# Kernel tuning notes

Hardware: AMD Instinct MI355X
Metric: run time of the kernel (lower is better)

## Reference

```python
import jax, jax.numpy as jnp
import numpy as np

N, E, G = 20000, 320000, 64
IN_DIM, HID, HEADS, NCLS = 512, 256, 2, 10
EPS = 1e-5
SLOPE = 0.2


def setup_inputs() -> dict:
    key = jax.random.key(0)
    ks = jax.random.split(key, 24)
    s = 0.02
    inp = {
        "feat": jax.random.normal(ks[0], (N, IN_DIM), jnp.float32),
        "src": jax.random.randint(ks[1], (E,), 0, N, jnp.int32),
        "dst": jax.random.randint(ks[2], (E,), 0, N, jnp.int32),
        "graph_ids": jnp.sort(jax.random.randint(ks[3], (N,), 0, G, jnp.int32)),
        # GATv2Conv params (fc_src, fc_dst, attn)
        "W_src": jax.random.normal(ks[4], (IN_DIM, HEADS * HID), jnp.float32) * s,
        "b_src": jnp.zeros((HEADS * HID,), jnp.float32),
        "W_dst": jax.random.normal(ks[5], (IN_DIM, HEADS * HID), jnp.float32) * s,
        "b_dst": jnp.zeros((HEADS * HID,), jnp.float32),
        "attn": jax.random.normal(ks[6], (HEADS, HID), jnp.float32) * s,
        # skip_lin: input_dim -> 2*hidden
        "W_skip": jax.random.normal(ks[7], (IN_DIM, 2 * HID), jnp.float32) * s,
        "b_skip": jnp.zeros((2 * HID,), jnp.float32),
        # bn1 affine
        "gamma": jnp.ones((2 * HID,), jnp.float32),
        "beta": jnp.zeros((2 * HID,), jnp.float32),
        # dim_reducer
        "W_red": jax.random.normal(ks[8], (2 * HID, HID), jnp.float32) * s,
        "b_red": jnp.zeros((HID,), jnp.float32),
        # attention-pool gate Linear(hidden, 1)
        "w_gate": jax.random.normal(ks[9], (HID, 1), jnp.float32) * s,
        "b_gate": jnp.zeros((1,), jnp.float32),
        # classifier MLP
        "W1": jax.random.normal(ks[10], (HID, HID // 2), jnp.float32) * s,
        "b1": jnp.zeros((HID // 2,), jnp.float32),
        "W2": jax.random.normal(ks[11], (HID // 2, NCLS), jnp.float32) * s,
        "b2": jnp.zeros((NCLS,), jnp.float32),
    }
    return inp


def _gatv2(feat, src, dst, W_src, b_src, W_dst, b_dst, attn):
    # feat_src/feat_dst: [N, H, D]
    fs = (feat @ W_src + b_src).reshape(N, HEADS, HID)
    fd = (feat @ W_dst + b_dst).reshape(N, HEADS, HID)
    fs_e = fs[src]                               # [E, H, D]
    m = jax.nn.leaky_relu(fs_e + fd[dst], SLOPE)  # [E, H, D]
    e = jnp.einsum("ehd,hd->eh", m, attn)         # [E, H]
    # edge softmax grouped by destination node
    e_max = jax.ops.segment_max(e, dst, num_segments=N)          # [N, H]
    e_exp = jnp.exp(e - e_max[dst])                               # [E, H]
    denom = jax.ops.segment_sum(e_exp, dst, num_segments=N)      # [N, H]
    alpha = e_exp / denom[dst]                                    # [E, H]
    out = jax.ops.segment_sum(alpha[:, :, None] * fs_e, dst, num_segments=N)
    return out  # [N, H, D]; zero rows for zero in-degree nodes


def reference(feat, src, dst, graph_ids, W_src, b_src, W_dst, b_dst, attn,
              W_skip, b_skip, gamma, beta, W_red, b_red, w_gate, b_gate,
              W1, b1, W2, b2):
    h1 = jax.nn.elu(_gatv2(feat, src, dst, W_src, b_src, W_dst, b_dst, attn))
    h1 = h1.reshape(N, HEADS * HID)
    h1 = h1 + (feat @ W_skip + b_skip)
    # BatchNorm1d (training-mode batch statistics, biased variance)
    mu = jnp.mean(h1, axis=0)
    var = jnp.mean((h1 - mu) ** 2, axis=0)
    h1 = (h1 - mu) * jax.lax.rsqrt(var + EPS) * gamma + beta
    hr = h1 @ W_red + b_red                      # [N, HID]
    # GlobalAttentionPooling: segment softmax of gate scores over each graph
    gate = hr @ w_gate + b_gate                  # [N, 1]
    g_max = jax.ops.segment_max(gate, graph_ids, num_segments=G)
    g_exp = jnp.exp(gate - g_max[graph_ids])
    g_den = jax.ops.segment_sum(g_exp, graph_ids, num_segments=G)
    a = g_exp / g_den[graph_ids]                 # [N, 1]
    h_g = jax.ops.segment_sum(a * hr, graph_ids, num_segments=G)  # [G, HID]
    # classifier (dropout = identity at inference)
    return jax.nn.relu(h_g @ W1 + b1) @ W2 + b2  # [G, NCLS]
```

## Files before the change

### kernel.cpp

```cpp
#include <hip/hip_runtime.h>
#include <math.h>

#define N_NODES 20000
#define N_EDGES 320000
#define N_GRAPH 64
#define IN_DIM  512
#define HID     256
#define F2      512
#define EPS_BN  1e-5f
#define SLOPE   0.2f
#define SCAN_BLOCKS 79
#define N_RT    157
#define RT_PAD  20096

#define SF_BLOCKS   5024
#define SW_BLOCKS   1024
#define INIT_BLOCKS 79
#define PREP_BLOCKS (SF_BLOCKS + SW_BLOCKS + INIT_BLOCKS)
#define TRIPLE_BLOCKS 1920
#define HIST_BLOCKS   1250

typedef unsigned short u16;
typedef __attribute__((ext_vector_type(8))) short bf16x8;
typedef __attribute__((ext_vector_type(4))) float floatx4;

__device__ __forceinline__ u16 bf_hi(float x) {
    unsigned int u = __float_as_uint(x);
    return (u16)((u + 0x7fffu + ((u >> 16) & 1u)) >> 16);
}
__device__ __forceinline__ float bf_val(u16 h) {
    return __uint_as_float((unsigned int)h << 16);
}
__device__ __forceinline__ void unpack2(unsigned int u, float& lo, float& hi) {
    lo = __uint_as_float(u << 16);
    hi = __uint_as_float(u & 0xffff0000u);
}
__device__ __forceinline__ float lr(float x) { return fmaxf(x, SLOPE * x); }

__global__ __launch_bounds__(256) void prep_kernel(
    const float* __restrict__ feat, u16* __restrict__ Fhi,
    const float* __restrict__ Ws, const float* __restrict__ Wd,
    const float* __restrict__ Wk, const float* __restrict__ Wr,
    u16* __restrict__ Whi, u16* __restrict__ Wlo,
    int* __restrict__ counts, int* __restrict__ cursor,
    float* __restrict__ stats, float* __restrict__ h_gnum,
    float* __restrict__ gden, float* __restrict__ gate) {
    __shared__ float t[32][33];
    int b = blockIdx.x;
    int tid = threadIdx.x;
    if (b < SF_BLOCKS) {
        int i = b * 256 + tid;
        size_t base = (size_t)i * 8;
        if (i >= N_NODES * IN_DIM / 8) {
            *(uint4*)(Fhi + base) = make_uint4(0, 0, 0, 0);
            return;
        }
        float4 x0 = *(const float4*)(feat + base);
        float4 x1 = *(const float4*)(feat + base + 4);
        float xs[8] = {x0.x, x0.y, x0.z, x0.w, x1.x, x1.y, x1.z, x1.w};
        union { u16 s[8]; uint4 v; } h;
#pragma unroll
        for (int j = 0; j < 8; j++) h.s[j] = bf_hi(xs[j]);
        *(uint4*)(Fhi + base) = h.v;
    } else if (b < SF_BLOCKS + SW_BLOCKS) {
        int bb = b - SF_BLOCKS;
        int kx = bb & 15, ny = (bb >> 4) & 15, w = bb >> 8;
        int ncols = (w == 3) ? 256 : 512;
        int n0 = ny * 32;
        if (n0 >= ncols) return;
        const float* W = (w == 0) ? Ws : ((w == 1) ? Wd : ((w == 2) ? Wk : Wr));
        size_t obase = (size_t)w * 512 * 512;
        int k0 = kx * 32;
        int tx = tid & 31, ty = tid >> 5;
#pragma unroll
        for (int i = 0; i < 4; i++)
            t[ty * 4 + i][tx] = W[(size_t)(k0 + ty * 4 + i) * ncols + n0 + tx];
        __syncthreads();
#pragma unroll
        for (int i = 0; i < 4; i++) {
            float x = t[tx][ty * 4 + i];
            u16 hh = bf_hi(x);
            size_t o = obase + (size_t)(n0 + ty * 4 + i) * 512 + k0 + tx;
            Whi[o] = hh;
            Wlo[o] = bf_hi(x - bf_val(hh));
        }
    } else {
        int i = (b - SF_BLOCKS - SW_BLOCKS) * 256 + tid;
        if (i < N_NODES) { counts[i] = 0; cursor[i] = 0; gate[i] = 0.f; }
        if (i < 1024) stats[i] = 0.f;
        if (i < N_GRAPH * HID) h_gnum[i] = 0.f;
        if (i < N_GRAPH) gden[i] = 0.f;
    }
}

__global__ __launch_bounds__(256) void gemm_mfma_triple(
    const u16* __restrict__ Fhi, const u16* __restrict__ Wthi,
    const float* __restrict__ b_src, const float* __restrict__ b_dst,
    const float* __restrict__ b_skip,
    u16* __restrict__ FS16, u16* __restrict__ FD16,
    u16* __restrict__ h1hi, u16* __restrict__ h1lo,
    const int* __restrict__ dst, int* __restrict__ counts) {
    __shared__ u16 As[2][128 * 72];
    int b = blockIdx.x;
    if (b >= TRIPLE_BLOCKS) {
        int e = (b - TRIPLE_BLOCKS) * 256 + threadIdx.x;
        if (e < N_EDGES) atomicAdd(&counts[dst[e]], 1);
        return;
    }
    int xcd = b & 7, slot = b >> 3;
    int rt = (slot / 12) * 8 + xcd;
    if (rt >= N_RT) return;
    int cw = slot % 12;
    int w_idx = cw >> 2;
    int col0 = (cw & 3) * 128;
    int row0 = rt * 128;
    int tid = threadIdx.x;
    int lane = tid & 63, wave = tid >> 6;
    int wm = (wave & 1) * 64, wn = (wave >> 1) * 64;
    int quad = lane >> 4, l16 = lane & 15;

    int sr = tid >> 1, sh = (tid & 1) * 32;
    const u16* gA = Fhi + (size_t)(row0 + sr) * 512 + sh;
    int sOff = sr * 72 + sh;

    const u16* Wb = Wthi + (size_t)w_idx * 512 * 512;
    const u16* bP[4];
#pragma unroll
    for (int nt = 0; nt < 4; nt++)
        bP[nt] = Wb + (size_t)(col0 + wn + nt * 16 + l16) * 512 + quad * 8;

    floatx4 acc[4][4];
#pragma unroll
    for (int i = 0; i < 4; i++)
#pragma unroll
        for (int j = 0; j < 4; j++) acc[i][j] = (floatx4){0.f, 0.f, 0.f, 0.f};

    union { uint4 u; bf16x8 v; } bcur[8], bnxt[8];
    {
        uint4 a0 = *(const uint4*)(gA + 0);
        uint4 a1 = *(const uint4*)(gA + 8);
        uint4 a2 = *(const uint4*)(gA + 16);
        uint4 a3 = *(const uint4*)(gA + 24);
#pragma unroll
        for (int nt = 0; nt < 4; nt++) {
            bcur[nt * 2 + 0].u = *(const uint4*)(bP[nt] + 0);
            bcur[nt * 2 + 1].u = *(const uint4*)(bP[nt] + 32);
        }
        *(uint4*)(&As[0][sOff + 0])  = a0;
        *(uint4*)(&As[0][sOff + 8])  = a1;
        *(uint4*)(&As[0][sOff + 16]) = a2;
        *(uint4*)(&As[0][sOff + 24]) = a3;
    }
    __syncthreads();

    for (int kk = 0; kk < 8; kk++) {
        uint4 na0, na1, na2, na3;
        bool more = kk < 7;
        if (more) {
            int k1 = (kk + 1) * 64;
            na0 = *(const uint4*)(gA + k1 + 0);
            na1 = *(const uint4*)(gA + k1 + 8);
            na2 = *(const uint4*)(gA + k1 + 16);
            na3 = *(const uint4*)(gA + k1 + 24);
#pragma unroll
            for (int nt = 0; nt < 4; nt++) {
                bnxt[nt * 2 + 0].u = *(const uint4*)(bP[nt] + k1 + 0);
                bnxt[nt * 2 + 1].u = *(const uint4*)(bP[nt] + k1 + 32);
            }
        }
        const u16* base = &As[kk & 1][0];
#pragma unroll
        for (int s = 0; s < 2; s++) {
#pragma unroll
            for (int mt = 0; mt < 4; mt++) {
                bf16x8 ah = *(const bf16x8*)&base[(wm + mt * 16 + l16) * 72 + s * 32 + quad * 8];
#pragma unroll
                for (int nt = 0; nt < 4; nt++)
                    acc[mt][nt] = __builtin_amdgcn_mfma_f32_16x16x32_bf16(
                        bcur[nt * 2 + s].v, ah, acc[mt][nt], 0, 0, 0);
            }
        }
        if (more) {
            u16* d = &As[(kk + 1) & 1][sOff];
            *(uint4*)(d + 0)  = na0;
            *(uint4*)(d + 8)  = na1;
            *(uint4*)(d + 16) = na2;
            *(uint4*)(d + 24) = na3;
            __syncthreads();
#pragma unroll
            for (int i = 0; i < 8; i++) bcur[i] = bnxt[i];
        }
    }

    const float* bias = (w_idx == 0) ? b_src : ((w_idx == 1) ? b_dst : b_skip);
    float4 b4[4];
#pragma unroll
    for (int wt = 0; wt < 4; wt++)
        b4[wt] = *(const float4*)(bias + col0 + wn + wt * 16 + quad * 4);
#pragma unroll
    for (int ft = 0; ft < 4; ft++) {
        int m = row0 + wm + ft * 16 + l16;
        if (m >= N_NODES) continue;
        size_t rb = (size_t)m * 512;
#pragma unroll
        for (int wt = 0; wt < 4; wt++) {
            int nb = col0 + wn + wt * 16 + quad * 4;
            float v0 = acc[ft][wt][0] + b4[wt].x;
            float v1 = acc[ft][wt][1] + b4[wt].y;
            float v2 = acc[ft][wt][2] + b4[wt].z;
            float v3 = acc[ft][wt][3] + b4[wt].w;
            u16 h0 = bf_hi(v0), h1_ = bf_hi(v1), h2 = bf_hi(v2), h3 = bf_hi(v3);
            uint2 wv;
            wv.x = (unsigned)h0 | ((unsigned)h1_ << 16);
            wv.y = (unsigned)h2 | ((unsigned)h3 << 16);
            if (w_idx == 0)      *(uint2*)(FS16 + rb + nb) = wv;
            else if (w_idx == 1) *(uint2*)(FD16 + rb + nb) = wv;
            else {
                *(uint2*)(h1hi + rb + nb) = wv;
                uint2 lv;
                lv.x = (unsigned)bf_hi(v0 - bf_val(h0)) | ((unsigned)bf_hi(v1 - bf_val(h1_)) << 16);
                lv.y = (unsigned)bf_hi(v2 - bf_val(h2)) | ((unsigned)bf_hi(v3 - bf_val(h3)) << 16);
                *(uint2*)(h1lo + rb + nb) = lv;
            }
        }
    }
}

__global__ __launch_bounds__(256) void scan_local_kernel(
    const int* __restrict__ counts, int* __restrict__ row_ptr, int* __restrict__ bsum) {
    __shared__ int buf[256];
    int b = blockIdx.x, tid = threadIdx.x;
    int i = b * 256 + tid;
    buf[tid] = (i < N_NODES) ? counts[i] : 0;
    __syncthreads();
    for (int off = 1; off < 256; off <<= 1) {
        int t = (tid >= off) ? buf[tid - off] : 0;
        __syncthreads();
        buf[tid] += t;
        __syncthreads();
    }
    if (i < N_NODES) row_ptr[i + 1] = buf[tid];
    if (tid == 255) bsum[b] = buf[255];
}

__global__ __launch_bounds__(256) void scan_fixup_kernel(
    const int* __restrict__ bsum, int* __restrict__ row_ptr) {
    __shared__ int red[256];
    int b = blockIdx.x, tid = threadIdx.x;
    red[tid] = (tid < b) ? bsum[tid] : 0;
    __syncthreads();
    for (int off = 128; off > 0; off >>= 1) {
        if (tid < off) red[tid] += red[tid + off];
        __syncthreads();
    }
    int offset = red[0];
    int i = b * 256 + tid;
    if (i < N_NODES) row_ptr[i + 1] += offset;
    if (b == 0 && tid == 0) row_ptr[0] = 0;
}

__global__ void scatter_kernel(const int* __restrict__ src, const int* __restrict__ dst,
                               const int* __restrict__ row_ptr,
                               int* __restrict__ cursor, int* __restrict__ csr_src) {
    int e = blockIdx.x * blockDim.x + threadIdx.x;
    if (e < N_EDGES) {
        int d = dst[e];
        int pos = atomicAdd(&cursor[d], 1);
        csr_src[row_ptr[d] + pos] = src[e];
    }
}

__global__ __launch_bounds__(256) void edge_fused_kernel(
    const u16* __restrict__ FS16, const u16* __restrict__ FD16,
    const float* __restrict__ attn, const int* __restrict__ csr_src,
    const int* __restrict__ row_ptr,
    u16* __restrict__ h1hi, u16* __restrict__ h1lo) {
    __shared__ float red[3 * 512];
    __shared__ float den[2];
    int n = blockIdx.x, tid = threadIdx.x;
    int lane = tid & 63, wave = tid >> 6;
    int beg = row_ptr[n], end = row_ptr[n + 1], deg = end - beg;
    if (tid < 2) den[tid] = 0.f;

    float fdv[8], aw[8];
    {
        uint4 q = *(const uint4*)(FD16 + (size_t)n * 512 + 8 * lane);
        unpack2(q.x, fdv[0], fdv[1]); unpack2(q.y, fdv[2], fdv[3]);
        unpack2(q.z, fdv[4], fdv[5]); unpack2(q.w, fdv[6], fdv[7]);
        float4 a0 = *(const float4*)(attn + 8 * lane);
        float4 a1 = *(const float4*)(attn + 8 * lane + 4);
        aw[0] = a0.x; aw[1] = a0.y; aw[2] = a0.z; aw[3] = a0.w;
        aw[4] = a1.x; aw[5] = a1.y; aw[6] = a1.z; aw[7] = a1.w;
    }
    __syncthreads();

    float acc[8] = {0.f, 0.f, 0.f, 0.f, 0.f, 0.f, 0.f, 0.f};
    float dp = 0.f;
    for (int j = wave; j < deg; j += 4) {
        int s = csr_src[beg + j];
        uint4 q = *(const uint4*)(FS16 + (size_t)s * 512 + 8 * lane);
        float f[8];
        unpack2(q.x, f[0], f[1]); unpack2(q.y, f[2], f[3]);
        unpack2(q.z, f[4], f[5]); unpack2(q.w, f[6], f[7]);
        float p = 0.f;
#pragma unroll
        for (int k = 0; k < 8; k++) p += lr(f[k] + fdv[k]) * aw[k];
#pragma unroll
        for (int off = 16; off > 0; off >>= 1) p += __shfl_xor(p, off, 64);
        float ex = expf(p);
#pragma unroll
        for (int k = 0; k < 8; k++) acc[k] += ex * f[k];
        if ((lane & 31) == 0) dp += ex;
    }
    if ((lane & 31) == 0) atomicAdd(&den[lane >> 5], dp);

    if (wave > 0) {
        float* r = &red[(wave - 1) * 512 + lane * 8];
        *(float4*)(r + 0) = *(float4*)&acc[0];
        *(float4*)(r + 4) = *(float4*)&acc[4];
    }
    __syncthreads();
    if (wave == 0) {
#pragma unroll
        for (int w = 0; w < 3; w++) {
            const float* r = &red[w * 512 + lane * 8];
#pragma unroll
            for (int k = 0; k < 8; k++) acc[k] += r[k];
        }
        float d = (lane < 32) ? den[0] : den[1];
        float inv = d > 0.f ? 1.f / d : 0.f;
        size_t base = (size_t)n * 512 + 8 * lane;
        union { u16 s[8]; uint4 v; } qh, ql;
        qh.v = *(const uint4*)(h1hi + base);
        ql.v = *(const uint4*)(h1lo + base);
#pragma unroll
        for (int k = 0; k < 8; k++) {
            float skip = bf_val(qh.s[k]) + bf_val(ql.s[k]);
            float x = acc[k] * inv;
            x = x > 0.f ? x : expm1f(x);
            float y = x + skip;
            u16 hh = bf_hi(y);
            qh.s[k] = hh;
            ql.s[k] = bf_hi(y - bf_val(hh));
        }
        *(uint4*)(h1hi + base) = qh.v;
        *(uint4*)(h1lo + base) = ql.v;
    }
}

__global__ __launch_bounds__(256) void bn_stats_kernel(const u16* __restrict__ h1hi,
                                                       float* __restrict__ stats,
                                                       int rows_per_block) {
    int tid = threadIdx.x;
    int r0 = blockIdx.x * rows_per_block;
    int r1 = min(r0 + rows_per_block, N_NODES);
    float s0 = 0.f, q0 = 0.f, s1 = 0.f, q1 = 0.f;
    for (int r = r0; r < r1; r++) {
        float a = bf_val(h1hi[(size_t)r * F2 + tid]);
        float b = bf_val(h1hi[(size_t)r * F2 + 256 + tid]);
        s0 += a; q0 += a * a;
        s1 += b; q1 += b * b;
    }
    atomicAdd(&stats[tid], s0);
    atomicAdd(&stats[256 + tid], s1);
    atomicAdd(&stats[512 + tid], q0);
    atomicAdd(&stats[512 + 256 + tid], q1);
}

__global__ __launch_bounds__(256) void bn_fold_kernel(
    const float* __restrict__ stats, const float* __restrict__ gamma,
    const float* __restrict__ beta,
    const u16* __restrict__ Whi3, const u16* __restrict__ Wlo3,
    const float* __restrict__ b_red,
    u16* __restrict__ Wphi, u16* __restrict__ Wplo, float* __restrict__ bias2) {
    __shared__ float sScale[512], sShift[512];
    __shared__ float red[256];
    int n = blockIdx.x, tid = threadIdx.x;
    for (int c = tid; c < 512; c += 256) {
        float mu = stats[c] / (float)N_NODES;
        float var = stats[512 + c] / (float)N_NODES - mu * mu;
        float sc = gamma[c] * rsqrtf(var + EPS_BN);
        sScale[c] = sc;
        sShift[c] = beta[c] - mu * sc;
    }
    __syncthreads();
    float part = 0.f;
    for (int k = tid; k < 512; k += 256) {
        size_t o = (size_t)n * 512 + k;
        float w = bf_val(Whi3[o]) + bf_val(Wlo3[o]);
        part += sShift[k] * w;
        float wp = w * sScale[k];
        u16 hh = bf_hi(wp);
        Wphi[o] = hh;
        Wplo[o] = bf_hi(wp - bf_val(hh));
    }
    red[tid] = part; __syncthreads();
    for (int off = 128; off > 0; off >>= 1) {
        if (tid < off) red[tid] += red[tid + off];
        __syncthreads();
    }
    if (tid == 0) bias2[n] = b_red[n] + red[0];
}

__global__ __launch_bounds__(256) void gemm_mfma_red(
    const u16* __restrict__ Ahi, const u16* __restrict__ Alo,
    const u16* __restrict__ Bhi, const u16* __restrict__ Blo,
    const float* __restrict__ bias2, const float* __restrict__ wg,
    float* __restrict__ hr, float* __restrict__ gate) {
    __shared__ u16 AsHi[128 * 40];
    __shared__ u16 AsLo[128 * 40];
    int tid = threadIdx.x;
    int row0 = blockIdx.x * 128;
    int col0 = blockIdx.y * 128;
    int lane = tid & 63, wave = tid >> 6;
    int wm = (wave & 1) * 64, wn = (wave >> 1) * 64;
    int quad = lane >> 4, l16 = lane & 15;

    int sr = tid >> 1, sh = (tid & 1) * 16;
    int grow = row0 + sr;
    bool ok = grow < N_NODES;
    u16* sH = &AsHi[sr * 40 + sh];
    u16* sL = &AsLo[sr * 40 + sh];

    const u16* bPh[4];
    const u16* bPl[4];
#pragma unroll
    for (int nt = 0; nt < 4; nt++) {
        size_t o = (size_t)(col0 + wn + nt * 16 + l16) * 512 + quad * 8;
        bPh[nt] = Bhi + o;
        bPl[nt] = Blo + o;
    }

    floatx4 acc[4][4];
#pragma unroll
    for (int i = 0; i < 4; i++)
#pragma unroll
        for (int j = 0; j < 4; j++) acc[i][j] = (floatx4){0.f, 0.f, 0.f, 0.f};

    for (int k0 = 0; k0 < 512; k0 += 32) {
        uint4 h0 = make_uint4(0, 0, 0, 0), h1v = h0, l0 = h0, l1 = h0;
        if (ok) {
            const u16* g = Ahi + (size_t)grow * 512 + k0 + sh;
            const u16* gl = Alo + (size_t)grow * 512 + k0 + sh;
            h0 = *(const uint4*)(g);
            h1v = *(const uint4*)(g + 8);
            l0 = *(const uint4*)(gl);
            l1 = *(const uint4*)(gl + 8);
        }
        union { uint4 u; bf16x8 v; } bh[4], bl[4];
#pragma unroll
        for (int nt = 0; nt < 4; nt++) {
            bh[nt].u = *(const uint4*)(bPh[nt] + k0);
            bl[nt].u = *(const uint4*)(bPl[nt] + k0);
        }
        __syncthreads();
        *(uint4*)(sH + 0) = h0;
        *(uint4*)(sH + 8) = h1v;
        *(uint4*)(sL + 0) = l0;
        *(uint4*)(sL + 8) = l1;
        __syncthreads();
#pragma unroll
        for (int mt = 0; mt < 4; mt++) {
            int me = (wm + mt * 16 + l16) * 40 + quad * 8;
            bf16x8 ah = *(const bf16x8*)&AsHi[me];
            bf16x8 al = *(const bf16x8*)&AsLo[me];
#pragma unroll
            for (int nt = 0; nt < 4; nt++) {
                acc[mt][nt] = __builtin_amdgcn_mfma_f32_16x16x32_bf16(bh[nt].v, ah, acc[mt][nt], 0, 0, 0);
                acc[mt][nt] = __builtin_amdgcn_mfma_f32_16x16x32_bf16(bl[nt].v, ah, acc[mt][nt], 0, 0, 0);
                acc[mt][nt] = __builtin_amdgcn_mfma_f32_16x16x32_bf16(bh[nt].v, al, acc[mt][nt], 0, 0, 0);
            }
        }
    }

    float4 b4[4], w4[4];
#pragma unroll
    for (int wt = 0; wt < 4; wt++) {
        int nb = col0 + wn + wt * 16 + quad * 4;
        b4[wt] = *(const float4*)(bias2 + nb);
        w4[wt] = *(const float4*)(wg + nb);
    }
#pragma unroll
    for (int ft = 0; ft < 4; ft++) {
        int m = row0 + wm + ft * 16 + l16;
        bool ok2 = m < N_NODES;
        float g = 0.f;
#pragma unroll
        for (int wt = 0; wt < 4; wt++) {
            float4 v;
            v.x = acc[ft][wt][0] + b4[wt].x;
            v.y = acc[ft][wt][1] + b4[wt].y;
            v.z = acc[ft][wt][2] + b4[wt].z;
            v.w = acc[ft][wt][3] + b4[wt].w;
            g += v.x * w4[wt].x + v.y * w4[wt].y + v.z * w4[wt].z + v.w * w4[wt].w;
            if (ok2) *(float4*)(hr + (size_t)m * HID + col0 + wn + wt * 16 + quad * 4) = v;
        }
        g += __shfl_xor(g, 16, 64);
        g += __shfl_xor(g, 32, 64);
        if (ok2 && lane < 16) atomicAdd(&gate[m], g);
    }
}

__device__ __forceinline__ int lower_bound_dev(const int* a, int n, int v) {
    int lo = 0, hi = n;
    while (lo < hi) {
        int mid = (lo + hi) >> 1;
        if (a[mid] < v) lo = mid + 1; else hi = mid;
    }
    return lo;
}

__global__ __launch_bounds__(256) void pool_partial_kernel(
    const float* __restrict__ hr, const float* __restrict__ gate,
    const int* __restrict__ gids, float* __restrict__ h_gnum,
    float* __restrict__ gden) {
    int b = blockIdx.x;
    int g = b >> 3, part = b & 7;
    int tid = threadIdx.x;
    int start = lower_bound_dev(gids, N_NODES, g);
    int end = lower_bound_dev(gids, N_NODES, g + 1);
    int span = end - start;
    int p_beg = start + (span * part) / 8;
    int p_end = start + (span * (part + 1)) / 8;
    if (p_beg >= p_end) return;
    __shared__ float wa[256];
    __shared__ float red[256];
    float acc = 0.f, denacc = 0.f;
    for (int cbeg = p_beg; cbeg < p_end; cbeg += 256) {
        int c = min(256, p_end - cbeg);
        float e = 0.f;
        if (tid < c) { e = expf(gate[cbeg + tid]); wa[tid] = e; }
        red[tid] = (tid < c) ? e : 0.f;
        __syncthreads();
        for (int off = 128; off > 0; off >>= 1) {
            if (tid < off) red[tid] += red[tid + off];
            __syncthreads();
        }
        denacc += red[0];
        for (int i = 0; i < c; i++) acc += wa[i] * hr[(size_t)(cbeg + i) * HID + tid];
        __syncthreads();
    }
    atomicAdd(&h_gnum[g * HID + tid], acc);
    if (tid == 0) atomicAdd(&gden[g], denacc);
}

__global__ __launch_bounds__(128) void classifier_kernel(
    const float* __restrict__ h_gnum, const float* __restrict__ gden,
    const float* __restrict__ W1, const float* __restrict__ b1,
    const float* __restrict__ W2, const float* __restrict__ b2,
    float* __restrict__ out) {
    int g = blockIdx.x;
    int tid = threadIdx.x;
    __shared__ float hg[256];
    __shared__ float z1[128];
    float d = gden[g];
    float invd = d > 0.f ? 1.f / d : 0.f;
    hg[tid] = h_gnum[g * HID + tid] * invd;
    hg[tid + 128] = h_gnum[g * HID + tid + 128] * invd;
    __syncthreads();
    float a = b1[tid];
#pragma unroll 8
    for (int k = 0; k < 256; k++) a += hg[k] * W1[k * 128 + tid];
    z1[tid] = a > 0.f ? a : 0.f;
    __syncthreads();
    if (tid < 10) {
        float o = b2[tid];
#pragma unroll 8
        for (int j = 0; j < 128; j++) o += z1[j] * W2[j * 10 + tid];
        out[g * 10 + tid] = o;
    }
}

extern "C" void kernel_launch(void* const* d_in, const int* in_sizes, int n_in,
                              void* d_out, int out_size, void* d_ws, size_t ws_size,
                              hipStream_t stream) {
    const float* feat   = (const float*)d_in[0];
    const int*   src    = (const int*)d_in[1];
    const int*   dst    = (const int*)d_in[2];
    const int*   gids   = (const int*)d_in[3];
    const float* W_src  = (const float*)d_in[4];
    const float* b_src  = (const float*)d_in[5];
    const float* W_dst  = (const float*)d_in[6];
    const float* b_dst  = (const float*)d_in[7];
    const float* attn   = (const float*)d_in[8];
    const float* W_skip = (const float*)d_in[9];
    const float* b_skip = (const float*)d_in[10];
    const float* gamma  = (const float*)d_in[11];
    const float* beta   = (const float*)d_in[12];
    const float* W_red  = (const float*)d_in[13];
    const float* b_red  = (const float*)d_in[14];
    const float* w_gate = (const float*)d_in[15];
    const float* W1     = (const float*)d_in[17];
    const float* b1     = (const float*)d_in[18];
    const float* W2     = (const float*)d_in[19];
    const float* b2     = (const float*)d_in[20];
    float* out = (float*)d_out;

    char* p = (char*)d_ws;
    auto alloc = [&](size_t bytes) -> char* {
        char* r = p;
        p += (bytes + 255) & ~(size_t)255;
        return r;
    };
    u16*   FS16     = (u16*)alloc((size_t)N_NODES * F2 * 2);
    u16*   FD16     = (u16*)alloc((size_t)N_NODES * F2 * 2);
    u16*   h1hi     = (u16*)alloc((size_t)N_NODES * F2 * 2);
    u16*   h1lo     = (u16*)alloc((size_t)N_NODES * F2 * 2);
    float* gate     = (float*)alloc((size_t)N_NODES * 4);
    float* stats    = (float*)alloc(1024 * 4);
    float* bias2    = (float*)alloc(256 * 4);
    float* h_gnum   = (float*)alloc((size_t)N_GRAPH * HID * 4);
    float* gden     = (float*)alloc((size_t)N_GRAPH * 4);
    int* counts     = (int*)alloc((size_t)N_NODES * 4);
    int* row_ptr    = (int*)alloc((size_t)(N_NODES + 1) * 4);
    int* cursor     = (int*)alloc((size_t)N_NODES * 4);
    int* csr_src    = (int*)alloc((size_t)N_EDGES * 4);
    int* bsum       = (int*)alloc((size_t)SCAN_BLOCKS * 4);
    u16* Fhi        = (u16*)alloc((size_t)RT_PAD * IN_DIM * 2);
    u16* Wthi       = (u16*)alloc((size_t)4 * 512 * 512 * 2);
    u16* Wtlo       = (u16*)alloc((size_t)4 * 512 * 512 * 2);
    u16* Wphi       = (u16*)alloc((size_t)HID * 512 * 2);
    u16* Wplo       = (u16*)alloc((size_t)HID * 512 * 2);
    float* hr = (float*)Fhi;
    (void)ws_size; (void)in_sizes; (void)n_in; (void)out_size;

    const size_t WSZ = (size_t)512 * 512;

    prep_kernel<<<PREP_BLOCKS, 256, 0, stream>>>(
        feat, Fhi, W_src, W_dst, W_skip, W_red, Wthi, Wtlo,
        counts, cursor, stats, h_gnum, gden, gate);

    gemm_mfma_triple<<<TRIPLE_BLOCKS + HIST_BLOCKS, 256, 0, stream>>>(
        Fhi, Wthi, b_src, b_dst, b_skip, FS16, FD16, h1hi, h1lo, dst, counts);

    scan_local_kernel<<<SCAN_BLOCKS, 256, 0, stream>>>(counts, row_ptr, bsum);
    scan_fixup_kernel<<<SCAN_BLOCKS, 256, 0, stream>>>(bsum, row_ptr);
    scatter_kernel<<<(N_EDGES + 255) / 256, 256, 0, stream>>>(src, dst, row_ptr, cursor, csr_src);

    edge_fused_kernel<<<N_NODES, 256, 0, stream>>>(
        FS16, FD16, attn, csr_src, row_ptr, h1hi, h1lo);

    bn_stats_kernel<<<500, 256, 0, stream>>>(h1hi, stats, 40);
    bn_fold_kernel<<<HID, 256, 0, stream>>>(
        stats, gamma, beta, Wthi + 3 * WSZ, Wtlo + 3 * WSZ, b_red, Wphi, Wplo, bias2);

    dim3 g256((N_NODES + 127) / 128, 2);
    gemm_mfma_red<<<g256, 256, 0, stream>>>(
        h1hi, h1lo, Wphi, Wplo, bias2, w_gate, hr, gate);

    pool_partial_kernel<<<N_GRAPH * 8, 256, 0, stream>>>(hr, gate, gids, h_gnum, gden);

    classifier_kernel<<<N_GRAPH, 128, 0, stream>>>(h_gnum, gden, W1, b1, W2, b2, out);
}
```

Before: 406.5 us.

## Stage GEMM A and B tiles into LDS via direct global_load_lds with XOR swizzle

The triple GEMM kernel now copies both the feature tile and the weight tile straight from global memory into LDS with the global_load_lds builtin, instead of routing A through registers and loading B directly into registers per wave. Both tiles use a 64-element-wide layout with an XOR swizzle to avoid bank conflicts, double-buffered across k-steps. This is meant to cut register pressure and VGPR round trips and to share B reuse across waves. In exchange, LDS use doubles and the barrier now sits at the end of each k-step, with no explicit wait on the asynchronous loads.

```diff
diff --git a/kernel.cpp b/kernel.cpp
--- a/kernel.cpp
+++ b/kernel.cpp
@@ -36,6 +36,12 @@
     hi = __uint_as_float(u & 0xffff0000u);
 }
 __device__ __forceinline__ float lr(float x) { return fmaxf(x, SLOPE * x); }
+
+__device__ __forceinline__ void gload16(const u16* g, u16* l) {
+    __builtin_amdgcn_global_load_lds(
+        (const __attribute__((address_space(1))) void*)g,
+        (__attribute__((address_space(3))) void*)l, 16, 0, 0);
+}
 
 __global__ __launch_bounds__(256) void prep_kernel(
     const float* __restrict__ feat, u16* __restrict__ Fhi,
@@ -100,7 +106,7 @@
     u16* __restrict__ FS16, u16* __restrict__ FD16,
     u16* __restrict__ h1hi, u16* __restrict__ h1lo,
     const int* __restrict__ dst, int* __restrict__ counts) {
-    __shared__ u16 As[2][128 * 72];
+    __shared__ u16 S[2][2][8192];
     int b = blockIdx.x;
     if (b >= TRIPLE_BLOCKS) {
         int e = (b - TRIPLE_BLOCKS) * 256 + threadIdx.x;
@@ -119,15 +125,28 @@
     int wm = (wave & 1) * 64, wn = (wave >> 1) * 64;
     int quad = lane >> 4, l16 = lane & 15;
 
-    int sr = tid >> 1, sh = (tid & 1) * 32;
-    const u16* gA = Fhi + (size_t)(row0 + sr) * 512 + sh;
-    int sOff = sr * 72 + sh;
-
-    const u16* Wb = Wthi + (size_t)w_idx * 512 * 512;
-    const u16* bP[4];
-#pragma unroll
-    for (int nt = 0; nt < 4; nt++)
-        bP[nt] = Wb + (size_t)(col0 + wn + nt * 16 + l16) * 512 + quad * 8;
+    int lrow = lane >> 3;
+    int kswz = ((lane & 7) ^ lrow) << 3;
+    const u16* aS = Fhi + (size_t)(row0 + wave * 32 + lrow) * 512 + kswz;
+    const u16* bS = Wthi + (size_t)w_idx * 512 * 512 +
+                    (size_t)(col0 + wave * 32 + lrow) * 512 + kswz;
+
+#define STAGE(buf, kk)                                                        \
+    do {                                                                      \
+        gload16(aS + (size_t)(kk) * 64,         &S[buf][0][(wave * 4 + 0) * 512]); \
+        gload16(bS + (size_t)(kk) * 64,         &S[buf][1][(wave * 4 + 0) * 512]); \
+        gload16(aS + 4096 + (size_t)(kk) * 64,  &S[buf][0][(wave * 4 + 1) * 512]); \
+        gload16(bS + 4096 + (size_t)(kk) * 64,  &S[buf][1][(wave * 4 + 1) * 512]); \
+        gload16(aS + 8192 + (size_t)(kk) * 64,  &S[buf][0][(wave * 4 + 2) * 512]); \
+        gload16(bS + 8192 + (size_t)(kk) * 64,  &S[buf][1][(wave * 4 + 2) * 512]); \
+        gload16(aS + 12288 + (size_t)(kk) * 64, &S[buf][0][(wave * 4 + 3) * 512]); \
+        gload16(bS + 12288 + (size_t)(kk) * 64, &S[buf][1][(wave * 4 + 3) * 512]); \
+    } while (0)
+
+    int kx8 = (l16 & 7) << 3;
+    int oS0 = (quad * 8) ^ kx8;
+    int offA = (wm + l16) * 64;
+    int offB = (wn + l16) * 64;
 
     floatx4 acc[4][4];
 #pragma unroll
@@ -135,62 +154,35 @@
 #pragma unroll
         for (int j = 0; j < 4; j++) acc[i][j] = (floatx4){0.f, 0.f, 0.f, 0.f};
 
-    union { uint4 u; bf16x8 v; } bcur[8], bnxt[8];
-    {
-        uint4 a0 = *(const uint4*)(gA + 0);
-        uint4 a1 = *(const uint4*)(gA + 8);
-        uint4 a2 = *(const uint4*)(gA + 16);
-        uint4 a3 = *(const uint4*)(gA + 24);
+    STAGE(0, 0);
+    __syncthreads();
+
+#pragma unroll
+    for (int kk = 0; kk < 8; kk++) {
+        if (kk < 7) STAGE((kk + 1) & 1, kk + 1);
+        const u16* A = &S[kk & 1][0][0];
+        const u16* B = &S[kk & 1][1][0];
+        bf16x8 bv[4][2];
 #pragma unroll
         for (int nt = 0; nt < 4; nt++) {
-            bcur[nt * 2 + 0].u = *(const uint4*)(bP[nt] + 0);
-            bcur[nt * 2 + 1].u = *(const uint4*)(bP[nt] + 32);
-        }
-        *(uint4*)(&As[0][sOff + 0])  = a0;
-        *(uint4*)(&As[0][sOff + 8])  = a1;
-        *(uint4*)(&As[0][sOff + 16]) = a2;
-        *(uint4*)(&As[0][sOff + 24]) = a3;
-    }
-    __syncthreads();
-
-    for (int kk = 0; kk < 8; kk++) {
-        uint4 na0, na1, na2, na3;
-        bool more = kk < 7;
-        if (more) {
-            int k1 = (kk + 1) * 64;
-            na0 = *(const uint4*)(gA + k1 + 0);
-            na1 = *(const uint4*)(gA + k1 + 8);
-            na2 = *(const uint4*)(gA + k1 + 16);
-            na3 = *(const uint4*)(gA + k1 + 24);
+            bv[nt][0] = *(const bf16x8*)&B[offB + nt * 1024 + oS0];
+            bv[nt][1] = *(const bf16x8*)&B[offB + nt * 1024 + (oS0 ^ 32)];
+        }
+#pragma unroll
+        for (int mt = 0; mt < 4; mt++) {
+            bf16x8 a0 = *(const bf16x8*)&A[offA + mt * 1024 + oS0];
+            bf16x8 a1 = *(const bf16x8*)&A[offA + mt * 1024 + (oS0 ^ 32)];
 #pragma unroll
             for (int nt = 0; nt < 4; nt++) {
-                bnxt[nt * 2 + 0].u = *(const uint4*)(bP[nt] + k1 + 0);
-                bnxt[nt * 2 + 1].u = *(const uint4*)(bP[nt] + k1 + 32);
+                acc[mt][nt] = __builtin_amdgcn_mfma_f32_16x16x32_bf16(
+                    bv[nt][0], a0, acc[mt][nt], 0, 0, 0);
+                acc[mt][nt] = __builtin_amdgcn_mfma_f32_16x16x32_bf16(
+                    bv[nt][1], a1, acc[mt][nt], 0, 0, 0);
             }
         }
-        const u16* base = &As[kk & 1][0];
-#pragma unroll
-        for (int s = 0; s < 2; s++) {
-#pragma unroll
-            for (int mt = 0; mt < 4; mt++) {
-                bf16x8 ah = *(const bf16x8*)&base[(wm + mt * 16 + l16) * 72 + s * 32 + quad * 8];
-#pragma unroll
-                for (int nt = 0; nt < 4; nt++)
-                    acc[mt][nt] = __builtin_amdgcn_mfma_f32_16x16x32_bf16(
-                        bcur[nt * 2 + s].v, ah, acc[mt][nt], 0, 0, 0);
-            }
-        }
-        if (more) {
-            u16* d = &As[(kk + 1) & 1][sOff];
-            *(uint4*)(d + 0)  = na0;
-            *(uint4*)(d + 8)  = na1;
-            *(uint4*)(d + 16) = na2;
-            *(uint4*)(d + 24) = na3;
-            __syncthreads();
-#pragma unroll
-            for (int i = 0; i < 8; i++) bcur[i] = bnxt[i];
-        }
-    }
+        __syncthreads();
+    }
+#undef STAGE
 
     const float* bias = (w_idx == 0) ? b_src : ((w_idx == 1) ? b_dst : b_skip);
     float4 b4[4];
```

Result: faster. 379.8 us (-6.6%).
